# Optimization experiments

Measured on AMD Instinct MI355X. Metric: run time of the kernel, lower is better.

## Reference

```python
import jax, jax.numpy as jnp
import numpy as np

B, S, D, H = 4, 2048, 1024, 16
DH = D // H  # head dim = 64


def setup_inputs() -> dict:
    key = jax.random.key(0)
    ks = jax.random.split(key, 7)
    q = jax.random.normal(ks[0], (B, S, D), dtype=jnp.float32)
    k = jax.random.normal(ks[1], (B, S, D), dtype=jnp.float32)
    v = jax.random.normal(ks[2], (B, S, D), dtype=jnp.float32)
    mask = jax.random.uniform(ks[3], (1, S, S), dtype=jnp.float32)
    sc = 1.0 / np.sqrt(D)
    Wq = jax.random.normal(ks[4], (D, D), dtype=jnp.float32) * sc
    Wk = jax.random.normal(ks[5], (D, D), dtype=jnp.float32) * sc
    Wv = jax.random.normal(ks[6], (D, D), dtype=jnp.float32) * sc
    return {"q": q, "k": k, "v": v, "mask": mask, "Wq": Wq, "Wk": Wk, "Wv": Wv}


def reference(q, k, v, mask, Wq, Wk, Wv):
    # Linear projections (no bias), then split hidden into H heads.
    # tf.concat(tf.split(x, H, axis=2), axis=0) == reshape to (B,S,H,DH);
    # the final split/concat restores channel order [head0, head1, ...],
    # i.e. a plain (B,S,H,DH)->(B,S,D) reshape.
    qh = (q @ Wq).reshape(B, S, H, DH)
    kh = (k @ Wk).reshape(B, S, H, DH)
    vh = (v @ Wv).reshape(B, S, H, DH)
    score = jnp.einsum("bqhd,bkhd->bhqk", qh, kh) / jnp.sqrt(
        jnp.asarray(DH, dtype=q.dtype))
    # multiplicative mask applied BEFORE softmax (broadcast (1,Sq,Sk))
    score = score * mask[:, None, :, :][0:1].squeeze(0) if False else score * mask  # mask (1,Sq,Sk) broadcasts over (B,H,Sq,Sk)
    attn = jax.nn.softmax(score, axis=-1)
    out = jnp.einsum("bhqk,bkhd->bqhd", attn, vh).reshape(B, S, D)
    return out
```

## Files before the change

### kernel.cpp

```cpp
#include <hip/hip_runtime.h>

#define B_  4
#define S_  2048
#define D_  1024
#define H_  16
#define DH_ 64

typedef __attribute__((ext_vector_type(8))) short bf16x8;
typedef __attribute__((ext_vector_type(4))) float f32x4;
typedef __attribute__((ext_vector_type(16))) float f32x16;
typedef __attribute__((ext_vector_type(4))) unsigned short u16x4;

__device__ __forceinline__ unsigned short f2bf(float f) {
  union { float f; unsigned int u; } x; x.f = f;
  unsigned int u = x.u;
  unsigned int r = (u + 0x7fffu + ((u >> 16) & 1u)) >> 16;
  return (unsigned short)r;
}

__device__ __forceinline__ int cvtpk(float lo, float hi) {
  unsigned r;
  asm("v_cvt_pk_bf16_f32 %0, %1, %2" : "=v"(r) : "v"(lo), "v"(hi));
  return (int)r;
}

__global__ __launch_bounds__(256) void wtrans_kernel(const float* __restrict__ W0,
                                                     const float* __restrict__ W1,
                                                     const float* __restrict__ W2,
                                                     unsigned short* __restrict__ Wt) {
  __shared__ float t[32][33];
  const int z = blockIdx.z;
  const float* W = (z == 0) ? W0 : ((z == 1) ? W1 : W2);
  unsigned short* O = Wt + (size_t)z * (D_ * D_);
  const int n0 = blockIdx.x * 32, k0 = blockIdx.y * 32;
  const int tx = threadIdx.x, ty = threadIdx.y;
#pragma unroll
  for (int i = 0; i < 4; i++) t[ty + i * 8][tx] = W[(size_t)(k0 + ty + i * 8) * D_ + n0 + tx];
  __syncthreads();
#pragma unroll
  for (int i = 0; i < 4; i++)
    O[(size_t)(n0 + ty + i * 8) * D_ + k0 + tx] = f2bf(t[tx][ty + i * 8]);
}

__global__ __launch_bounds__(256) void proj_kernel(const float* __restrict__ X0,
                                                   const float* __restrict__ X1,
                                                   const float* __restrict__ X2,
                                                   const unsigned short* __restrict__ Wt,
                                                   unsigned short* __restrict__ Y0) {
  __shared__ unsigned short Alds[128 * 72];
  __shared__ unsigned short Blds[128 * 72];
  const int z = blockIdx.z;
  const float* X = (z == 0) ? X0 : ((z == 1) ? X1 : X2);
  const unsigned short* Wz = Wt + (size_t)z * (D_ * D_);
  unsigned short* Y = Y0 + (size_t)z * ((size_t)B_ * S_ * D_);
  const float osc = (z == 0) ? 0.18033688f : 1.0f;

  const int tid = threadIdx.x;
  const int lane = tid & 63, w = tid >> 6;
  const int wr = w >> 1, wc = w & 1;
  const int l15 = lane & 15, lg = lane >> 4;
  const int r0 = blockIdx.y * 128, c0 = blockIdx.x * 128;

  f32x4 acc[4][4];
#pragma unroll
  for (int m = 0; m < 4; m++)
#pragma unroll
    for (int n = 0; n < 4; n++) acc[m][n] = (f32x4){0.f, 0.f, 0.f, 0.f};

  for (int kt = 0; kt < 16; ++kt) {
    __syncthreads();
    {
      const int rr = tid >> 4, cf = (tid & 15) * 4;
#pragma unroll
      for (int p = 0; p < 8; p++) {
        int row = rr + p * 16;
        float4 xv = *(const float4*)(X + (size_t)(r0 + row) * D_ + kt * 64 + cf);
        u16x4 bb = { f2bf(xv.x), f2bf(xv.y), f2bf(xv.z), f2bf(xv.w) };
        *(u16x4*)(&Alds[row * 72 + cf]) = bb;
      }
      const int rb = tid >> 3, cb = tid & 7;
#pragma unroll
      for (int p = 0; p < 4; p++) {
        int row = rb + p * 32;
        bf16x8 wv = *(const bf16x8*)(Wz + (size_t)(c0 + row) * D_ + kt * 64 + cb * 8);
        *(bf16x8*)(&Blds[row * 72 + cb * 8]) = wv;
      }
    }
    __syncthreads();

    bf16x8 af[4][2];
#pragma unroll
    for (int m = 0; m < 4; m++)
#pragma unroll
      for (int kc = 0; kc < 2; kc++)
        af[m][kc] = *(const bf16x8*)(&Alds[(wr * 64 + m * 16 + l15) * 72 + kc * 32 + lg * 8]);
#pragma unroll
    for (int n = 0; n < 4; n++) {
      bf16x8 bfr[2];
#pragma unroll
      for (int kc = 0; kc < 2; kc++)
        bfr[kc] = *(const bf16x8*)(&Blds[(wc * 64 + n * 16 + l15) * 72 + kc * 32 + lg * 8]);
#pragma unroll
      for (int m = 0; m < 4; m++)
#pragma unroll
        for (int kc = 0; kc < 2; kc++)
          acc[m][n] = __builtin_amdgcn_mfma_f32_16x16x32_bf16(af[m][kc], bfr[kc], acc[m][n], 0, 0, 0);
    }
  }

#pragma unroll
  for (int m = 0; m < 4; m++)
#pragma unroll
    for (int n = 0; n < 4; n++)
#pragma unroll
      for (int r = 0; r < 4; r++) {
        int row = r0 + wr * 64 + m * 16 + lg * 4 + r;
        int col = c0 + wc * 64 + n * 16 + l15;
        Y[(size_t)row * D_ + col] = f2bf(acc[m][n][r] * osc);
      }
}

__global__ __launch_bounds__(256) void attn_kernel(
    const unsigned short* __restrict__ qh,
    const unsigned short* __restrict__ kh,
    const unsigned short* __restrict__ vh,
    const float* __restrict__ mask,
    float* __restrict__ out) {
  __shared__ __align__(16) unsigned short K_lds[2][64 * 72];
  __shared__ __align__(16) unsigned short V_lds[2][64 * 72];

  const int tid = threadIdx.x;
  const int lane = tid & 63, w = tid >> 6;
  const int l31 = lane & 31, hf = lane >> 5;
  const int q0 = blockIdx.x * 128;
  const int h = blockIdx.y, b = blockIdx.z;
  const size_t head = (size_t)b * S_ * D_ + h * DH_;
  const int qrow = q0 + w * 32 + l31;

  bf16x8 bq[4];
  {
    const unsigned short* qp = qh + head + (size_t)qrow * D_;
#pragma unroll
    for (int ds = 0; ds < 4; ds++) bq[ds] = *(const bf16x8*)(qp + ds * 16 + hf * 8);
  }

  const int rr = tid >> 3, cc = tid & 7;
  const unsigned short* kbase = kh + head + (size_t)rr * D_ + cc * 8;
  const unsigned short* vbase = vh + head + (size_t)rr * D_ + cc * 8;

  f32x16 o_acc[2];
#pragma unroll
  for (int dt = 0; dt < 2; dt++)
#pragma unroll
    for (int r = 0; r < 16; r++) o_acc[dt][r] = 0.f;
  float m_r = -INFINITY, l_r = 0.f;

  {
#pragma unroll
    for (int p = 0; p < 2; p++) {
      bf16x8 kreg = *(const bf16x8*)(kbase + (size_t)p * 32 * D_);
      bf16x8 vreg = *(const bf16x8*)(vbase + (size_t)p * 32 * D_);
      int row = rr + p * 32;
      *(bf16x8*)(&K_lds[0][row * 72 + cc * 8]) = kreg;
#pragma unroll
      for (int j = 0; j < 8; j++) {
        int d = cc * 8 + j;
        int byt = (d * 72 + row) * 2;
        byt ^= ((d >> 3) & 7) << 4;
        *(unsigned short*)((char*)&V_lds[0][0] + byt) = (unsigned short)vreg[j];
      }
    }
    __syncthreads();
  }

  for (int kt = 0; kt < 32; kt++) {
    const int cur = kt & 1;
    const bool more = (kt + 1 < 32);

    const size_t tb = (size_t)(more ? kt + 1 : kt) * 64 * D_;
    bf16x8 kreg2[2], vreg2[2];
#pragma unroll
    for (int p = 0; p < 2; p++) {
      kreg2[p] = *(const bf16x8*)(kbase + tb + (size_t)p * 32 * D_);
      vreg2[p] = *(const bf16x8*)(vbase + tb + (size_t)p * 32 * D_);
    }
    __builtin_amdgcn_sched_barrier(0);

    f32x16 sacc[2];
#pragma unroll
    for (int ct = 0; ct < 2; ct++)
#pragma unroll
      for (int r = 0; r < 16; r++) sacc[ct][r] = 0.f;
    __builtin_amdgcn_s_setprio(1);
#pragma unroll
    for (int ds = 0; ds < 4; ds++)
#pragma unroll
      for (int ct = 0; ct < 2; ct++) {
        bf16x8 ak = *(const bf16x8*)(&K_lds[cur][(ct * 32 + l31) * 72 + ds * 16 + hf * 8]);
        sacc[ct] = __builtin_amdgcn_mfma_f32_32x32x16_bf16(ak, bq[ds], sacc[ct], 0, 0, 0);
      }
    __builtin_amdgcn_s_setprio(0);

    const float* mrow = mask + (size_t)qrow * S_ + kt * 64 + hf * 4;
#pragma unroll
    for (int ct = 0; ct < 2; ct++)
#pragma unroll
      for (int rq = 0; rq < 4; rq++) {
        float4 mk = *(const float4*)(mrow + ct * 32 + rq * 8);
        sacc[ct][rq * 4 + 0] *= mk.x;
        sacc[ct][rq * 4 + 1] *= mk.y;
        sacc[ct][rq * 4 + 2] *= mk.z;
        sacc[ct][rq * 4 + 3] *= mk.w;
      }

    float red[16];
#pragma unroll
    for (int i = 0; i < 16; i++) red[i] = fmaxf(sacc[0][i], sacc[1][i]);
#pragma unroll
    for (int off = 8; off >= 1; off >>= 1)
#pragma unroll
      for (int i = 0; i < off; i++) red[i] = fmaxf(red[i], red[i + off]);
    float tm = fmaxf(red[0], __shfl_xor(red[0], 32));

    float mn;
    if (__any(tm > m_r + 8.0f)) {
      mn = fmaxf(m_r, tm);
      float alpha = exp2f(m_r - mn);
      m_r = mn;
      l_r *= alpha;
#pragma unroll
      for (int dt = 0; dt < 2; dt++)
#pragma unroll
        for (int r = 0; r < 16; r++) o_acc[dt][r] *= alpha;
    } else {
      mn = m_r;
    }

#pragma unroll
    for (int ct = 0; ct < 2; ct++)
#pragma unroll
      for (int r = 0; r < 16; r++) sacc[ct][r] = exp2f(sacc[ct][r] - mn);

    float sr[16];
#pragma unroll
    for (int i = 0; i < 16; i++) sr[i] = sacc[0][i] + sacc[1][i];
#pragma unroll
    for (int off = 8; off >= 1; off >>= 1)
#pragma unroll
      for (int i = 0; i < off; i++) sr[i] += sr[i + off];
    l_r += sr[0] + __shfl_xor(sr[0], 32);

    bf16x8 bfp[4];
#pragma unroll
    for (int s = 0; s < 4; s++) {
      const int ct = s >> 1, rb = (s & 1) * 8;
      int L1 = cvtpk(sacc[ct][rb + 0], sacc[ct][rb + 1]);
      int L2 = cvtpk(sacc[ct][rb + 2], sacc[ct][rb + 3]);
      int H1 = cvtpk(sacc[ct][rb + 4], sacc[ct][rb + 5]);
      int H2 = cvtpk(sacc[ct][rb + 6], sacc[ct][rb + 7]);
      int xL1 = __shfl_xor(L1, 32), xL2 = __shfl_xor(L2, 32);
      int xH1 = __shfl_xor(H1, 32), xH2 = __shfl_xor(H2, 32);
      union { int u[4]; bf16x8 v; } cv;
      cv.u[0] = hf ? xH1 : L1;
      cv.u[1] = hf ? xH2 : L2;
      cv.u[2] = hf ? H1 : xL1;
      cv.u[3] = hf ? H2 : xL2;
      bfp[s] = cv.v;
    }

    __builtin_amdgcn_s_setprio(1);
#pragma unroll
    for (int dt = 0; dt < 2; dt++) {
      const int d0 = dt * 32 + l31;
      const int bbase = d0 * 144;
      const int swz = ((d0 >> 3) & 7) << 4;
#pragma unroll
      for (int s = 0; s < 4; s++) {
        int byt = (bbase + (s * 16 + hf * 8) * 2) ^ swz;
        bf16x8 av = *(const bf16x8*)((const char*)&V_lds[cur][0] + byt);
        o_acc[dt] = __builtin_amdgcn_mfma_f32_32x32x16_bf16(av, bfp[s], o_acc[dt], 0, 0, 0);
      }
    }
    __builtin_amdgcn_s_setprio(0);

    if (more) {
#pragma unroll
      for (int p = 0; p < 2; p++) {
        int row = rr + p * 32;
        *(bf16x8*)(&K_lds[cur ^ 1][row * 72 + cc * 8]) = kreg2[p];
#pragma unroll
        for (int j = 0; j < 8; j++) {
          int d = cc * 8 + j;
          int byt = (d * 72 + row) * 2;
          byt ^= ((d >> 3) & 7) << 4;
          *(unsigned short*)((char*)&V_lds[cur ^ 1][0] + byt) = (unsigned short)vreg2[p][j];
        }
      }
      __syncthreads();
    }
  }

  const float invl = 1.0f / l_r;
  float* op = out + (size_t)(b * S_ + qrow) * D_ + h * DH_;
#pragma unroll
  for (int dt = 0; dt < 2; dt++)
#pragma unroll
    for (int rq = 0; rq < 4; rq++) {
      float4 ov = { o_acc[dt][rq * 4 + 0] * invl, o_acc[dt][rq * 4 + 1] * invl,
                    o_acc[dt][rq * 4 + 2] * invl, o_acc[dt][rq * 4 + 3] * invl };
      *(float4*)(op + dt * 32 + rq * 8 + hf * 4) = ov;
    }
}

extern "C" void kernel_launch(void* const* d_in, const int* in_sizes, int n_in,
                              void* d_out, int out_size, void* d_ws, size_t ws_size,
                              hipStream_t stream) {
  const float* q = (const float*)d_in[0];
  const float* k = (const float*)d_in[1];
  const float* v = (const float*)d_in[2];
  const float* mask = (const float*)d_in[3];
  const float* Wq = (const float*)d_in[4];
  const float* Wk = (const float*)d_in[5];
  const float* Wv = (const float*)d_in[6];

  char* ws = (char*)d_ws;
  const size_t SZ_PROJ = (size_t)B_ * S_ * D_ * 2;
  unsigned short* qh = (unsigned short*)(ws);
  unsigned short* kh = (unsigned short*)(ws + SZ_PROJ);
  unsigned short* vh = (unsigned short*)(ws + 2 * SZ_PROJ);
  unsigned short* Wt = (unsigned short*)(ws + 3 * SZ_PROJ);

  wtrans_kernel<<<dim3(D_ / 32, D_ / 32, 3), dim3(32, 8), 0, stream>>>(Wq, Wk, Wv, Wt);
  proj_kernel<<<dim3(D_ / 128, (B_ * S_) / 128, 3), 256, 0, stream>>>(q, k, v, Wt, qh);
  attn_kernel<<<dim3(S_ / 128, H_, B_), 256, 0, stream>>>(qh, kh, vh, mask, (float*)d_out);
}
```

Before: 333.6 us.

## Write V projection pre-transposed per head so attention loads V with vector stores

The projection kernel now writes the V output as [B,H,DH,S] by staging the tile transposed in shared memory and storing 16-byte chunks. The attention kernel then reads V rows along S and writes them to LDS with one swizzled 16-byte store per chunk, replacing eight scalar 2-byte transposing stores per chunk. This moves the V transpose out of the attention kernel's inner loop into the projection epilogue, at the cost of an extra LDS round trip and two barriers in the projection kernel for the V slice.

```diff
diff --git a/kernel.cpp b/kernel.cpp
--- a/kernel.cpp
+++ b/kernel.cpp
@@ -47,8 +47,9 @@
                                                    const float* __restrict__ X2,
                                                    const unsigned short* __restrict__ Wt,
                                                    unsigned short* __restrict__ Y0) {
-  __shared__ unsigned short Alds[128 * 72];
-  __shared__ unsigned short Blds[128 * 72];
+  __shared__ __align__(16) unsigned short smem[2 * 128 * 72];
+  unsigned short* Alds = smem;
+  unsigned short* Blds = smem + 128 * 72;
   const int z = blockIdx.z;
   const float* X = (z == 0) ? X0 : ((z == 1) ? X1 : X2);
   const unsigned short* Wz = Wt + (size_t)z * (D_ * D_);
@@ -108,22 +109,44 @@
     }
   }
 
-#pragma unroll
-  for (int m = 0; m < 4; m++)
-#pragma unroll
-    for (int n = 0; n < 4; n++)
-#pragma unroll
-      for (int r = 0; r < 4; r++) {
-        int row = r0 + wr * 64 + m * 16 + lg * 4 + r;
-        int col = c0 + wc * 64 + n * 16 + l15;
-        Y[(size_t)row * D_ + col] = f2bf(acc[m][n][r] * osc);
-      }
+  if (z == 2) {
+    __syncthreads();
+#pragma unroll
+    for (int m = 0; m < 4; m++)
+#pragma unroll
+      for (int n = 0; n < 4; n++)
+#pragma unroll
+        for (int r = 0; r < 4; r++) {
+          int srow = wr * 64 + m * 16 + lg * 4 + r;
+          int dcol = wc * 64 + n * 16 + l15;
+          smem[dcol * 136 + srow] = f2bf(acc[m][n][r]);
+        }
+    __syncthreads();
+    const int dl = tid >> 1, sh = (tid & 1) * 64;
+    const int bb = r0 >> 11, s0 = r0 & 2047;
+    const int hh = (c0 + dl) >> 6, dd = (c0 + dl) & 63;
+    size_t gbase = ((size_t)(bb * H_ + hh) * DH_ + dd) * (size_t)S_ + s0 + sh;
+#pragma unroll
+    for (int j = 0; j < 8; j++)
+      *(bf16x8*)(Y + gbase + j * 8) = *(const bf16x8*)(&smem[dl * 136 + sh + j * 8]);
+  } else {
+#pragma unroll
+    for (int m = 0; m < 4; m++)
+#pragma unroll
+      for (int n = 0; n < 4; n++)
+#pragma unroll
+        for (int r = 0; r < 4; r++) {
+          int row = r0 + wr * 64 + m * 16 + lg * 4 + r;
+          int col = c0 + wc * 64 + n * 16 + l15;
+          Y[(size_t)row * D_ + col] = f2bf(acc[m][n][r] * osc);
+        }
+  }
 }
 
 __global__ __launch_bounds__(256) void attn_kernel(
     const unsigned short* __restrict__ qh,
     const unsigned short* __restrict__ kh,
-    const unsigned short* __restrict__ vh,
+    const unsigned short* __restrict__ vt,
     const float* __restrict__ mask,
     float* __restrict__ out) {
   __shared__ __align__(16) unsigned short K_lds[2][64 * 72];
@@ -146,7 +169,7 @@
 
   const int rr = tid >> 3, cc = tid & 7;
   const unsigned short* kbase = kh + head + (size_t)rr * D_ + cc * 8;
-  const unsigned short* vbase = vh + head + (size_t)rr * D_ + cc * 8;
+  const unsigned short* vtb = vt + ((size_t)(b * H_ + h) * DH_ + rr) * (size_t)S_ + cc * 8;
 
   f32x16 o_acc[2];
 #pragma unroll
@@ -159,16 +182,11 @@
 #pragma unroll
     for (int p = 0; p < 2; p++) {
       bf16x8 kreg = *(const bf16x8*)(kbase + (size_t)p * 32 * D_);
-      bf16x8 vreg = *(const bf16x8*)(vbase + (size_t)p * 32 * D_);
+      bf16x8 vreg = *(const bf16x8*)(vtb + (size_t)p * 32 * S_);
       int row = rr + p * 32;
       *(bf16x8*)(&K_lds[0][row * 72 + cc * 8]) = kreg;
-#pragma unroll
-      for (int j = 0; j < 8; j++) {
-        int d = cc * 8 + j;
-        int byt = (d * 72 + row) * 2;
-        byt ^= ((d >> 3) & 7) << 4;
-        *(unsigned short*)((char*)&V_lds[0][0] + byt) = (unsigned short)vreg[j];
-      }
+      int byt = (row * 144 + cc * 16) ^ (((row >> 3) & 7) << 4);
+      *(bf16x8*)((char*)&V_lds[0][0] + byt) = vreg;
     }
     __syncthreads();
   }
@@ -177,12 +195,12 @@
     const int cur = kt & 1;
     const bool more = (kt + 1 < 32);
 
-    const size_t tb = (size_t)(more ? kt + 1 : kt) * 64 * D_;
+    const int ktn = more ? kt + 1 : kt;
     bf16x8 kreg2[2], vreg2[2];
 #pragma unroll
     for (int p = 0; p < 2; p++) {
-      kreg2[p] = *(const bf16x8*)(kbase + tb + (size_t)p * 32 * D_);
-      vreg2[p] = *(const bf16x8*)(vbase + tb + (size_t)p * 32 * D_);
+      kreg2[p] = *(const bf16x8*)(kbase + (size_t)ktn * 64 * D_ + (size_t)p * 32 * D_);
+      vreg2[p] = *(const bf16x8*)(vtb + (size_t)ktn * 64 + (size_t)p * 32 * S_);
     }
     __builtin_amdgcn_sched_barrier(0);
 
@@ -288,13 +306,8 @@
       for (int p = 0; p < 2; p++) {
         int row = rr + p * 32;
         *(bf16x8*)(&K_lds[cur ^ 1][row * 72 + cc * 8]) = kreg2[p];
-#pragma unroll
-        for (int j = 0; j < 8; j++) {
-          int d = cc * 8 + j;
-          int byt = (d * 72 + row) * 2;
-          byt ^= ((d >> 3) & 7) << 4;
-          *(unsigned short*)((char*)&V_lds[cur ^ 1][0] + byt) = (unsigned short)vreg2[p][j];
-        }
+        int byt = (row * 144 + cc * 16) ^ (((row >> 3) & 7) << 4);
+        *(bf16x8*)((char*)&V_lds[cur ^ 1][0] + byt) = vreg2[p];
       }
       __syncthreads();
     }
@@ -327,10 +340,10 @@
   const size_t SZ_PROJ = (size_t)B_ * S_ * D_ * 2;
   unsigned short* qh = (unsigned short*)(ws);
   unsigned short* kh = (unsigned short*)(ws + SZ_PROJ);
-  unsigned short* vh = (unsigned short*)(ws + 2 * SZ_PROJ);
+  unsigned short* vhT = (unsigned short*)(ws + 2 * SZ_PROJ);
   unsigned short* Wt = (unsigned short*)(ws + 3 * SZ_PROJ);
 
   wtrans_kernel<<<dim3(D_ / 32, D_ / 32, 3), dim3(32, 8), 0, stream>>>(Wq, Wk, Wv, Wt);
   proj_kernel<<<dim3(D_ / 128, (B_ * S_) / 128, 3), 256, 0, stream>>>(q, k, v, Wt, qh);
-  attn_kernel<<<dim3(S_ / 128, H_, B_), 256, 0, stream>>>(qh, kh, vh, mask, (float*)d_out);
-}
+  attn_kernel<<<dim3(S_ / 128, H_, B_), 256, 0, stream>>>(qh, kh, vhT, mask, (float*)d_out);
+}
```

Measured after the change: 335.0 us. About the same (+0.4%).
